# Optimization experiments

Hardware: AMD Instinct MI355X
Metric: run time of the kernel (lower is better)

The kernel has to match this reference:

```python
import jax, jax.numpy as jnp
import numpy as np

N = 100000
E = 1600000
H = 2   # heads
C = 64  # per-head channels
NEG_SLOPE = 0.2


def setup_inputs() -> dict:
    key = jax.random.key(0)
    ks = jax.random.split(key, 12)
    s = 0.05
    return {
        "logits": jax.random.normal(ks[0], (N, 40), jnp.float32),
        "features": jax.random.normal(ks[1], (N, 256), jnp.float32),
        "edge_index": jax.random.randint(ks[2], (2, E), 0, N, jnp.int32),
        "W_feat": jax.random.normal(ks[3], (256, 128), jnp.float32) * s,
        "b_feat": jnp.zeros((128,), jnp.float32),
        "W0": jax.random.normal(ks[4], (168, 128), jnp.float32) * s,
        "att_src0": jax.random.normal(ks[5], (H, C), jnp.float32) * s,
        "att_dst0": jax.random.normal(ks[6], (H, C), jnp.float32) * s,
        "bias0": jnp.zeros((128,), jnp.float32),
        "W1": jax.random.normal(ks[7], (128, 128), jnp.float32) * s,
        "att_src1": jax.random.normal(ks[8], (H, C), jnp.float32) * s,
        "att_dst1": jax.random.normal(ks[9], (H, C), jnp.float32) * s,
        "bias1": jnp.zeros((128,), jnp.float32),
        "W_out": jax.random.normal(ks[10], (128, 40), jnp.float32) * s,
        "b_out": jnp.zeros((40,), jnp.float32),
    }


def gat_conv(x, src, dst, W, att_src, att_dst, bias):
    # x: [N, F_in] -> h: [N, H, C]
    h = (x @ W).reshape(N, H, C)
    a_src = (h * att_src).sum(-1)  # [N, H]
    a_dst = (h * att_dst).sum(-1)  # [N, H]
    # per-edge attention logits, leaky relu
    e = jax.nn.leaky_relu(a_src[src] + a_dst[dst], NEG_SLOPE)  # [E+N, H]
    # segment softmax over incoming edges of each dst node
    e_max = jax.ops.segment_max(e, dst, num_segments=N)
    e_exp = jnp.exp(e - e_max[dst])
    denom = jax.ops.segment_sum(e_exp, dst, num_segments=N)
    alpha = e_exp / (denom[dst] + 1e-16)  # [E+N, H]
    # weighted message aggregation (scatter-add)
    msg = h[src] * alpha[:, :, None]  # [E+N, H, C]
    out = jax.ops.segment_sum(msg, dst, num_segments=N)
    return out.reshape(N, H * C) + bias


def reference(logits, features, edge_index, W_feat, b_feat,
              W0, att_src0, att_dst0, bias0,
              W1, att_src1, att_dst1, bias1,
              W_out, b_out):
    # input assembly: [logits | proj(features)]
    x = jnp.concatenate([logits, features @ W_feat + b_feat], axis=-1)  # [N,168]
    # add self loops (PyG GATConv default add_self_loops=True)
    loops = jnp.arange(N, dtype=edge_index.dtype)
    src = jnp.concatenate([edge_index[0], loops])
    dst = jnp.concatenate([edge_index[1], loops])
    x = gat_conv(x, src, dst, W0, att_src0, att_dst0, bias0)
    x = jax.nn.relu(x)  # relu between conv layers (dropout=0 / eval)
    x = gat_conv(x, src, dst, W1, att_src1, att_dst1, bias1)
    return x @ W_out + b_out  # [N, 40]
```

## Files before the change

### kernel.cpp

```cpp
#include <hip/hip_runtime.h>

#define NN 100000
#define EE 1600000
#define NBUCK ((NN + 255) >> 8)
#define CHUNK 8192
#define NPBLK ((EE + CHUNK - 1) / CHUNK)

typedef __attribute__((ext_vector_type(8))) short short8_t;
typedef __attribute__((ext_vector_type(4))) float f32x4;

static __device__ inline unsigned short f2bf(float f) {
    unsigned int u = __float_as_uint(f);
    u += 0x7FFFu + ((u >> 16) & 1u);
    return (unsigned short)(u >> 16);
}
static __device__ inline float bf2f(unsigned short h) {
    return __uint_as_float(((unsigned int)h) << 16);
}

__global__ __launch_bounds__(256) void part_count(const int* __restrict__ ei,
                                                  int* __restrict__ cnt) {
    __shared__ int h[NBUCK];
    for (int i = threadIdx.x; i < NBUCK; i += 256) h[i] = 0;
    __syncthreads();
    int e0 = blockIdx.x * CHUNK;
    int e1 = e0 + CHUNK; if (e1 > EE) e1 = EE;
    for (int e = e0 + threadIdx.x; e < e1; e += 256)
        atomicAdd(&h[ei[EE + e] >> 8], 1);
    __syncthreads();
    for (int i = threadIdx.x; i < NBUCK; i += 256)
        cnt[blockIdx.x * NBUCK + i] = h[i];
}

__global__ void part_scan(const int* __restrict__ cnt, int* __restrict__ base,
                          int* __restrict__ bbase) {
    __shared__ int tot[512];
    int b = threadIdx.x;
    int t = 0;
    if (b < NBUCK)
        for (int k = 0; k < NPBLK; ++k) t += cnt[k * NBUCK + b];
    tot[b] = t;
    __syncthreads();
    for (int off = 1; off < 512; off <<= 1) {
        int u = (b >= off) ? tot[b - off] : 0;
        __syncthreads();
        tot[b] += u;
        __syncthreads();
    }
    int excl = tot[b] - t;
    if (b < NBUCK) {
        bbase[b] = excl;
        int run = excl;
        for (int k = 0; k < NPBLK; ++k) {
            base[k * NBUCK + b] = run;
            run += cnt[k * NBUCK + b];
        }
    }
    if (b == 0) bbase[NBUCK] = EE;
}

__global__ __launch_bounds__(256) void part_scatter(const int* __restrict__ ei,
                                                    const int* __restrict__ base,
                                                    unsigned int* __restrict__ bbuf) {
    __shared__ int lcur[NBUCK];
    for (int i = threadIdx.x; i < NBUCK; i += 256)
        lcur[i] = base[blockIdx.x * NBUCK + i];
    __syncthreads();
    int e0 = blockIdx.x * CHUNK;
    int e1 = e0 + CHUNK; if (e1 > EE) e1 = EE;
    for (int e = e0 + threadIdx.x; e < e1; e += 256) {
        int s = ei[e], d = ei[EE + e];
        int pos = atomicAdd(&lcur[d >> 8], 1);
        bbuf[pos] = (unsigned int)s | ((unsigned int)(d & 255) << 24);
    }
}

__global__ __launch_bounds__(256) void csr_build(const unsigned int* __restrict__ bbuf,
                                                 const int* __restrict__ bbase,
                                                 int* __restrict__ row_ptr,
                                                 int* __restrict__ col) {
    __shared__ int hist[256];
    __shared__ int sc[256];
    __shared__ int lcur[256];
    int b = blockIdx.x;
    int t = threadIdx.x;
    int n0 = b << 8;
    int nCnt = NN - n0; if (nCnt > 256) nCnt = 256;
    int es = bbase[b], ee2 = bbase[b + 1];
    hist[t] = 0;
    __syncthreads();
    for (int i = es + t; i < ee2; i += 256)
        atomicAdd(&hist[bbuf[i] >> 24], 1);
    __syncthreads();
    int v = hist[t];
    sc[t] = v;
    __syncthreads();
    for (int off = 1; off < 256; off <<= 1) {
        int u = (t >= off) ? sc[t - off] : 0;
        __syncthreads();
        sc[t] += u;
        __syncthreads();
    }
    int excl = sc[t] - v;
    if (t < nCnt) row_ptr[n0 + t] = es + excl;
    if (b == 0 && t == 0) row_ptr[NN] = EE;
    lcur[t] = excl;
    __syncthreads();
    for (int i = es + t; i < ee2; i += 256) {
        unsigned int pk = bbuf[i];
        int lpos = atomicAdd(&lcur[pk >> 24], 1);
        col[es + lpos] = (int)(pk & 0x00FFFFFFu);
    }
}

__global__ void bsplit_kernel(const float* __restrict__ W, int ldw, int K, int N,
                              unsigned short* __restrict__ BThi,
                              unsigned short* __restrict__ BTlo,
                              int stride, int koff, int KPseg) {
    int k = blockIdx.x * 256 + threadIdx.x;
    int col = blockIdx.y;
    if (k >= KPseg) return;
    float v = (k < K && col < N) ? W[(size_t)k * ldw + col] : 0.f;
    unsigned short hi = f2bf(v);
    unsigned short lo = f2bf(v - bf2f(hi));
    BThi[(size_t)col * stride + koff + k] = hi;
    BTlo[(size_t)col * stride + koff + k] = lo;
}

__global__ void cvec_kernel(const float* __restrict__ b_feat,
                            const float* __restrict__ W0, float* __restrict__ cvec) {
    int j = threadIdx.x;
    float s = 0.f;
    for (int k = 0; k < 128; ++k) s += b_feat[k] * W0[(40 + k) * 128 + j];
    cvec[j] = s;
}

#define AHI 0
#define ALO 2048
#define BHI 4096
#define BLO 8192
template <int OUTBF16, int ABF16, int ATTN, int NCT>
__global__ __launch_bounds__(256) void mfma_gemm_kernel(
    const void* __restrict__ A1v, int lda1, int K1, int KP1,
    const float* __restrict__ A2, int lda2, int K2,
    int M,
    const unsigned short* __restrict__ BThi, const unsigned short* __restrict__ BTlo,
    int bstride, int KPtot,
    void* __restrict__ Cout, int ldc, int Nact, const float* __restrict__ bias,
    const float* __restrict__ att_src, const float* __restrict__ att_dst,
    float* __restrict__ a_srcO, float* __restrict__ a_dstO)
{
    __shared__ __align__(16) unsigned short lds[12288];
    const int t = threadIdx.x;
    const int w = t >> 6, lane = t & 63;
    const int row0 = blockIdx.x * 64;
    const int rbase = (w & 1) * 32;
    const int cbase = (NCT == 4) ? (w >> 1) * 64 : (w >> 1) * 32;

    f32x4 acc[2][NCT];
#pragma unroll
    for (int i = 0; i < 2; ++i)
#pragma unroll
        for (int j = 0; j < NCT; ++j) acc[i][j] = (f32x4){0.f, 0.f, 0.f, 0.f};

    const int arow = t >> 2;
    const int aslot = t & 3;
    const bool rowok = (row0 + arow) < M;
    const int aoff = arow * 32 + (((aslot ^ ((arow >> 1) & 3))) << 3);

    const int bc0 = t >> 2,         bs0 = t & 3;
    const int bc1 = (t + 256) >> 2, bs1 = (t + 256) & 3;
    const int bo0 = bc0 * 32 + ((bs0 ^ ((bc0 >> 1) & 3)) << 3);
    const int bo1 = bc1 * 32 + ((bs1 ^ ((bc1 >> 1) & 3)) << 3);

    float ra0[8], ra1[8];
    short8_t rab0, rab1;
    short8_t bh0a, bl0a, bh1a, bl1a;
    short8_t bh0b, bl0b, bh1b, bl1b;
    const short8_t zz = {0, 0, 0, 0, 0, 0, 0, 0};

#define LOADB_(k0_, H0, L0, H1, L1) {                                     \
        size_t g0_ = (size_t)bc0 * bstride + (k0_) + bs0 * 8;             \
        H0 = *(const short8_t*)&BThi[g0_];                                \
        L0 = *(const short8_t*)&BTlo[g0_];                                \
        if (NCT == 4) {                                                   \
            size_t g1_ = (size_t)bc1 * bstride + (k0_) + bs1 * 8;         \
            H1 = *(const short8_t*)&BThi[g1_];                            \
            L1 = *(const short8_t*)&BTlo[g1_];                            \
        }                                                                 \
    }

#define LOADA_(k0_, RA, RAB) {                                            \
        if (ABF16) {                                                      \
            int gk = (k0_) + aslot * 8;                                   \
            if (rowok && gk + 8 <= K1) {                                  \
                const unsigned short* Ab =                                \
                    (const unsigned short*)A1v + (size_t)(row0 + arow) * lda1; \
                RAB = *(const short8_t*)&Ab[gk];                          \
            } else RAB = zz;                                              \
        } else {                                                          \
            const float* Asrc; int gk, Klim;                              \
            if ((k0_) < KP1) {                                            \
                Asrc = (const float*)A1v + (size_t)(row0 + arow) * lda1;  \
                gk = (k0_) + aslot * 8; Klim = K1;                        \
            } else {                                                      \
                Asrc = A2 + (size_t)(row0 + arow) * lda2;                 \
                gk = (k0_) - KP1 + aslot * 8; Klim = K2;                  \
            }                                                             \
            if (rowok && gk + 8 <= Klim) {                                \
                float4 v0 = *(const float4*)(Asrc + gk);                  \
                float4 v1 = *(const float4*)(Asrc + gk + 4);              \
                RA[0] = v0.x; RA[1] = v0.y; RA[2] = v0.z; RA[3] = v0.w;   \
                RA[4] = v1.x; RA[5] = v1.y; RA[6] = v1.z; RA[7] = v1.w;   \
            } else {                                                      \
                for (int j_ = 0; j_ < 8; ++j_) RA[j_] = 0.f;              \
            }                                                             \
        }                                                                 \
    }

#define STAGE_(RA, RAB, H0, L0, H1, L1) {                                 \
        if (ABF16) {                                                      \
            *(short8_t*)&lds[AHI + aoff] = RAB;                           \
        } else {                                                          \
            short8_t vh_, vl_;                                            \
            for (int j_ = 0; j_ < 8; ++j_) {                              \
                unsigned short hi_ = f2bf(RA[j_]);                        \
                vh_[j_] = (short)hi_;                                     \
                vl_[j_] = (short)f2bf(RA[j_] - bf2f(hi_));                \
            }                                                             \
            *(short8_t*)&lds[AHI + aoff] = vh_;                           \
            *(short8_t*)&lds[ALO + aoff] = vl_;                           \
        }                                                                 \
        *(short8_t*)&lds[BHI + bo0] = H0;                                 \
        *(short8_t*)&lds[BLO + bo0] = L0;                                 \
        if (NCT == 4) {                                                   \
            *(short8_t*)&lds[BHI + bo1] = H1;                             \
            *(short8_t*)&lds[BLO + bo1] = L1;                             \
        }                                                                 \
    }

#define COMPUTE_() {                                                      \
        short8_t Ah[2], Al[2], Bh[NCT], Bl[NCT];                          \
        const int fslot = lane >> 4;                                      \
        for (int rt = 0; rt < 2; ++rt) {                                  \
            int r = rbase + rt * 16 + (lane & 15);                        \
            int off = r * 32 + ((fslot ^ ((r >> 1) & 3)) << 3);           \
            Ah[rt] = *(const short8_t*)&lds[AHI + off];                   \
            if (!ABF16) Al[rt] = *(const short8_t*)&lds[ALO + off];       \
        }                                                                 \
        for (int ct = 0; ct < NCT; ++ct) {                                \
            int c = cbase + ct * 16 + (lane & 15);                        \
            int off = c * 32 + ((fslot ^ ((c >> 1) & 3)) << 3);           \
            Bh[ct] = *(const short8_t*)&lds[BHI + off];                   \
            Bl[ct] = *(const short8_t*)&lds[BLO + off];                   \
        }                                                                 \
        for (int rt = 0; rt < 2; ++rt)                                    \
            for (int ct = 0; ct < NCT; ++ct) {                            \
                acc[rt][ct] = __builtin_amdgcn_mfma_f32_16x16x32_bf16(Ah[rt], Bh[ct], acc[rt][ct], 0, 0, 0); \
                acc[rt][ct] = __builtin_amdgcn_mfma_f32_16x16x32_bf16(Ah[rt], Bl[ct], acc[rt][ct], 0, 0, 0); \
                if (!ABF16)                                               \
                    acc[rt][ct] = __builtin_amdgcn_mfma_f32_16x16x32_bf16(Al[rt], Bh[ct], acc[rt][ct], 0, 0, 0); \
            }                                                             \
    }

    LOADA_(0, ra0, rab0);
    LOADB_(0, bh0a, bl0a, bh1a, bl1a);
    LOADA_(32, ra1, rab1);
    LOADB_(32, bh0b, bl0b, bh1b, bl1b);

    for (int k0 = 0; k0 < KPtot; k0 += 64) {
        STAGE_(ra0, rab0, bh0a, bl0a, bh1a, bl1a);
        __syncthreads();
        if (k0 + 64 < KPtot) {
            LOADA_(k0 + 64, ra0, rab0);
            LOADB_(k0 + 64, bh0a, bl0a, bh1a, bl1a);
        }
        COMPUTE_();
        __syncthreads();

        STAGE_(ra1, rab1, bh0b, bl0b, bh1b, bl1b);
        __syncthreads();
        if (k0 + 96 < KPtot) {
            LOADA_(k0 + 96, ra1, rab1);
            LOADB_(k0 + 96, bh0b, bl0b, bh1b, bl1b);
        }
        COMPUTE_();
        __syncthreads();
    }

#pragma unroll
    for (int rt = 0; rt < 2; ++rt) {
#pragma unroll
        for (int reg = 0; reg < 4; ++reg) {
            int r = row0 + rbase + rt * 16 + (lane >> 4) * 4 + reg;
            if (ATTN) {
                float ps = 0.f, pd = 0.f;
#pragma unroll
                for (int ct = 0; ct < NCT; ++ct) {
                    int c = cbase + ct * 16 + (lane & 15);
                    ps += acc[rt][ct][reg] * att_src[c];
                    pd += acc[rt][ct][reg] * att_dst[c];
                }
#pragma unroll
                for (int off = 1; off < 16; off <<= 1) {
                    ps += __shfl_xor(ps, off);
                    pd += __shfl_xor(pd, off);
                }
                if (r < M && (lane & 15) == 0) {
                    int head = w >> 1;
                    a_srcO[r * 2 + head] = ps;
                    a_dstO[r * 2 + head] = pd;
                }
            }
            if (r >= M) continue;
#pragma unroll
            for (int ct = 0; ct < NCT; ++ct) {
                int c = cbase + ct * 16 + (lane & 15);
                float v = acc[rt][ct][reg];
                if (bias) v += bias[c];
                if (OUTBF16) {
                    ((unsigned short*)Cout)[(size_t)r * 128 + c] = f2bf(v);
                } else {
                    if (c < Nact)
                        ((float*)Cout)[(size_t)r * ldc + c] = v;
                }
            }
        }
    }
#undef LOADA_
#undef LOADB_
#undef STAGE_
#undef COMPUTE_
}

template <int RELU, int OUTBF16>
__global__ void gat_agg_fused(const int* __restrict__ row_ptr, const int* __restrict__ col,
                              const float* __restrict__ a_src, const float* __restrict__ a_dst,
                              const unsigned short* __restrict__ hb,
                              const float* __restrict__ bias, void* __restrict__ out) {
    int wid = (blockIdx.x * 256 + threadIdx.x) >> 6;
    if (wid >= NN) return;
    int lane = threadIdx.x & 63;
    int hc = lane >> 5;
    const unsigned int* h2 = (const unsigned int*)hb;

    float2 ad = ((const float2*)a_dst)[wid];
    float2 asf = ((const float2*)a_src)[wid];
    float adh = hc ? ad.y : ad.x;
    float e0 = (hc ? asf.y : asf.x) + adh;
    e0 = e0 > 0.f ? e0 : 0.2f * e0;
    float w = __expf(e0);
    unsigned int hv = h2[wid * 64 + lane];
    float accx = w * __uint_as_float(hv << 16);
    float accy = w * __uint_as_float(hv & 0xFFFF0000u);
    float den = w;
    const int shbase = hc << 5;

    int rs = row_ptr[wid], re = row_ptr[wid + 1];
    for (int base = rs; base < re; base += 32) {
        int cnt = re - base;
        if (cnt > 32) cnt = 32;
        int eidx = lane & 31;
        int sL = 0;
        float wL = 0.f;
        if (eidx < cnt) {
            sL = col[base + eidx];
            float2 as = ((const float2*)a_src)[sL];
            float tt = (hc ? as.y : as.x) + adh;
            tt = tt > 0.f ? tt : 0.2f * tt;
            wL = __expf(tt);
        }
        int i = 0;
        for (; i + 8 <= cnt; i += 8) {
            int s[8];
            unsigned int g[8];
            float ws[8];
#pragma unroll
            for (int j = 0; j < 8; ++j) s[j] = __shfl(sL, shbase + i + j);
#pragma unroll
            for (int j = 0; j < 8; ++j) g[j] = h2[s[j] * 64 + lane];
#pragma unroll
            for (int j = 0; j < 8; ++j) ws[j] = __shfl(wL, shbase + i + j);
#pragma unroll
            for (int j = 0; j < 8; ++j) {
                accx += ws[j] * __uint_as_float(g[j] << 16);
                accy += ws[j] * __uint_as_float(g[j] & 0xFFFF0000u);
                den += ws[j];
            }
        }
        for (; i + 4 <= cnt; i += 4) {
            int s[4];
            unsigned int g[4];
            float ws[4];
#pragma unroll
            for (int j = 0; j < 4; ++j) s[j] = __shfl(sL, shbase + i + j);
#pragma unroll
            for (int j = 0; j < 4; ++j) g[j] = h2[s[j] * 64 + lane];
#pragma unroll
            for (int j = 0; j < 4; ++j) ws[j] = __shfl(wL, shbase + i + j);
#pragma unroll
            for (int j = 0; j < 4; ++j) {
                accx += ws[j] * __uint_as_float(g[j] << 16);
                accy += ws[j] * __uint_as_float(g[j] & 0xFFFF0000u);
                den += ws[j];
            }
        }
        for (; i < cnt; ++i) {
            int s = __shfl(sL, shbase + i);
            float ws = __shfl(wL, shbase + i);
            unsigned int hs = h2[s * 64 + lane];
            accx += ws * __uint_as_float(hs << 16);
            accy += ws * __uint_as_float(hs & 0xFFFF0000u);
            den += ws;
        }
    }
    float inv = 1.f / (den + 1e-16f);
    float2 b2 = ((const float2*)bias)[lane];
    float ox = accx * inv + b2.x;
    float oy = accy * inv + b2.y;
    if (RELU) { ox = fmaxf(ox, 0.f); oy = fmaxf(oy, 0.f); }
    if (OUTBF16) {
        unsigned int pk = (unsigned int)f2bf(ox) | ((unsigned int)f2bf(oy) << 16);
        ((unsigned int*)out)[wid * 64 + lane] = pk;
    } else {
        ((float2*)out)[wid * 64 + lane] = make_float2(ox, oy);
    }
}

extern "C" void kernel_launch(void* const* d_in, const int* in_sizes, int n_in,
                              void* d_out, int out_size, void* d_ws, size_t ws_size,
                              hipStream_t stream) {
    const float* logits   = (const float*)d_in[0];
    const float* features = (const float*)d_in[1];
    const int*   ei       = (const int*)d_in[2];
    const float* W_feat   = (const float*)d_in[3];
    const float* b_feat   = (const float*)d_in[4];
    const float* W0       = (const float*)d_in[5];
    const float* att_src0 = (const float*)d_in[6];
    const float* att_dst0 = (const float*)d_in[7];
    const float* bias0    = (const float*)d_in[8];
    const float* W1       = (const float*)d_in[9];
    const float* att_src1 = (const float*)d_in[10];
    const float* att_dst1 = (const float*)d_in[11];
    const float* bias1    = (const float*)d_in[12];
    const float* W_out    = (const float*)d_in[13];
    const float* b_out    = (const float*)d_in[14];
    float* out = (float*)d_out;

    float* agg    = (float*)d_ws;
    float* a_srcb = agg + (size_t)NN * 128;
    float* a_dstb = a_srcb + (size_t)NN * 2;
    float* Wc     = a_dstb + (size_t)NN * 2;
    float* cvec   = Wc + 256 * 128;
    unsigned short* hbuf = (unsigned short*)(cvec + 128);
    unsigned short* BT0hi = hbuf + (size_t)NN * 128;
    unsigned short* BT0lo = BT0hi + 128 * 320;
    unsigned short* BTbhi = BT0lo + 128 * 320;
    unsigned short* BTblo = BTbhi + 128 * 128;
    unsigned short* BT1hi = BTblo + 128 * 128;
    unsigned short* BT1lo = BT1hi + 128 * 128;
    unsigned short* BTohi = BT1lo + 128 * 128;
    unsigned short* BTolo = BTohi + 128 * 128;
    int* row_ptr = (int*)(BTolo + 128 * 128);
    int* colbuf  = row_ptr + NN + 1;
    int* cnt     = colbuf + EE;
    int* pbase   = cnt + NPBLK * NBUCK;
    int* bbase   = pbase + NPBLK * NBUCK;
    unsigned int* bbuf = (unsigned int*)agg;
    unsigned short* aggb = (unsigned short*)agg;

    dim3 blk(256);
    const int gemmGrid = (NN + 63) / 64;
    const int nodeWaveGrid = (NN + 3) / 4;

    part_count<<<dim3(NPBLK), blk, 0, stream>>>(ei, cnt);
    part_scan<<<dim3(1), dim3(512), 0, stream>>>(cnt, pbase, bbase);
    part_scatter<<<dim3(NPBLK), blk, 0, stream>>>(ei, pbase, bbuf);
    csr_build<<<dim3(NBUCK), blk, 0, stream>>>(bbuf, bbase, row_ptr, colbuf);

    bsplit_kernel<<<dim3(1, 128), blk, 0, stream>>>(W0, 128, 40, 128, BT0hi, BT0lo, 320, 0, 64);
    bsplit_kernel<<<dim3(1, 128), blk, 0, stream>>>(W0 + 40 * 128, 128, 128, 128, BTbhi, BTblo, 128, 0, 128);
    mfma_gemm_kernel<0, 0, 0, 4><<<dim3(4), blk, 0, stream>>>(
        W_feat, 128, 128, 128, nullptr, 0, 0, 256,
        BTbhi, BTblo, 128, 128, Wc, 128, 128, nullptr,
        nullptr, nullptr, nullptr, nullptr);
    cvec_kernel<<<dim3(1), dim3(128), 0, stream>>>(b_feat, W0, cvec);
    bsplit_kernel<<<dim3(1, 128), blk, 0, stream>>>(Wc, 128, 256, 128, BT0hi, BT0lo, 320, 64, 256);
    bsplit_kernel<<<dim3(1, 128), blk, 0, stream>>>(W1, 128, 128, 128, BT1hi, BT1lo, 128, 0, 128);
    bsplit_kernel<<<dim3(1, 128), blk, 0, stream>>>(W_out, 40, 128, 40, BTohi, BTolo, 128, 0, 128);

    mfma_gemm_kernel<1, 0, 1, 4><<<dim3(gemmGrid), blk, 0, stream>>>(
        logits, 40, 40, 64, features, 256, 256, NN,
        BT0hi, BT0lo, 320, 320, hbuf, 128, 128, cvec,
        att_src0, att_dst0, a_srcb, a_dstb);
    gat_agg_fused<1, 1><<<dim3(nodeWaveGrid), blk, 0, stream>>>(
        row_ptr, colbuf, a_srcb, a_dstb, hbuf, bias0, aggb);

    mfma_gemm_kernel<1, 1, 1, 4><<<dim3(gemmGrid), blk, 0, stream>>>(
        aggb, 128, 128, 128, nullptr, 0, 0, NN,
        BT1hi, BT1lo, 128, 128, hbuf, 128, 128, nullptr,
        att_src1, att_dst1, a_srcb, a_dstb);
    gat_agg_fused<0, 0><<<dim3(nodeWaveGrid), blk, 0, stream>>>(
        row_ptr, colbuf, a_srcb, a_dstb, hbuf, bias1, agg);

    mfma_gemm_kernel<0, 0, 0, 2><<<dim3(gemmGrid), blk, 0, stream>>>(
        agg, 128, 128, 128, nullptr, 0, 0, NN,
        BTohi, BTolo, 128, 128, out, 40, 40, b_out,
        nullptr, nullptr, nullptr, nullptr);
}
```

Baseline: 316.2 us.

## Drop LDS staging in GEMM and process two nodes per wave in aggregation

The MFMA GEMM loses its shared-memory staging and block barriers. Each wave now loads its A and B fragments straight from global memory into registers, owns a 32-row by 64-column tile, and double-buffers A across k-steps. The GAT aggregation kernel now handles two nodes per wave with 32 lanes each, reading 4 bf16 per lane and loop bounds set by the larger degree of the pair. The aim is to remove barrier and LDS overhead and to raise memory-level parallelism, at the cost of redundant global B reads across waves and idle lanes when paired nodes have very different degrees.

```diff
diff --git a/kernel.cpp b/kernel.cpp
--- a/kernel.cpp
+++ b/kernel.cpp
@@ -17,6 +17,7 @@
 static __device__ inline float bf2f(unsigned short h) {
     return __uint_as_float(((unsigned int)h) << 16);
 }
+static __device__ inline float u2f(unsigned int u) { return __uint_as_float(u); }
 
 __global__ __launch_bounds__(256) void part_count(const int* __restrict__ ei,
                                                   int* __restrict__ cnt) {
@@ -135,11 +136,7 @@
     cvec[j] = s;
 }
 
-#define AHI 0
-#define ALO 2048
-#define BHI 4096
-#define BLO 8192
-template <int OUTBF16, int ABF16, int ATTN, int NCT>
+template <int OUTBF16, int ABF16, int ATTN, int NCT, int COLSPLIT>
 __global__ __launch_bounds__(256) void mfma_gemm_kernel(
     const void* __restrict__ A1v, int lda1, int K1, int KP1,
     const float* __restrict__ A2, int lda2, int K2,
@@ -150,12 +147,14 @@
     const float* __restrict__ att_src, const float* __restrict__ att_dst,
     float* __restrict__ a_srcO, float* __restrict__ a_dstO)
 {
-    __shared__ __align__(16) unsigned short lds[12288];
-    const int t = threadIdx.x;
-    const int w = t >> 6, lane = t & 63;
-    const int row0 = blockIdx.x * 64;
-    const int rbase = (w & 1) * 32;
-    const int cbase = (NCT == 4) ? (w >> 1) * 64 : (w >> 1) * 32;
+    const int wv = (blockIdx.x * 256 + threadIdx.x) >> 6;
+    const int nRowWaves = M >> 5;
+    if (wv >= nRowWaves * COLSPLIT) return;
+    const int lane = threadIdx.x & 63;
+    const int fr = lane & 15;
+    const int fslot = lane >> 4;
+    const int row0 = (COLSPLIT == 2 ? (wv >> 1) : wv) * 32;
+    const int cbase = (COLSPLIT == 2 ? (wv & 1) * 64 : 0);
 
     f32x4 acc[2][NCT];
 #pragma unroll
@@ -163,141 +162,107 @@
 #pragma unroll
         for (int j = 0; j < NCT; ++j) acc[i][j] = (f32x4){0.f, 0.f, 0.f, 0.f};
 
-    const int arow = t >> 2;
-    const int aslot = t & 3;
-    const bool rowok = (row0 + arow) < M;
-    const int aoff = arow * 32 + (((aslot ^ ((arow >> 1) & 3))) << 3);
-
-    const int bc0 = t >> 2,         bs0 = t & 3;
-    const int bc1 = (t + 256) >> 2, bs1 = (t + 256) & 3;
-    const int bo0 = bc0 * 32 + ((bs0 ^ ((bc0 >> 1) & 3)) << 3);
-    const int bo1 = bc1 * 32 + ((bs1 ^ ((bc1 >> 1) & 3)) << 3);
-
-    float ra0[8], ra1[8];
-    short8_t rab0, rab1;
-    short8_t bh0a, bl0a, bh1a, bl1a;
-    short8_t bh0b, bl0b, bh1b, bl1b;
+    const unsigned short* Bhp[NCT];
+    const unsigned short* Blp[NCT];
+#pragma unroll
+    for (int ct = 0; ct < NCT; ++ct) {
+        size_t co = (size_t)(cbase + ct * 16 + fr) * bstride;
+        Bhp[ct] = BThi + co;
+        Blp[ct] = BTlo + co;
+    }
+    const unsigned short* Arow_b[2] = {nullptr, nullptr};
+    if (ABF16) {
+        Arow_b[0] = (const unsigned short*)A1v + (size_t)(row0 + fr) * lda1;
+        Arow_b[1] = Arow_b[0] + (size_t)16 * lda1;
+    }
+
     const short8_t zz = {0, 0, 0, 0, 0, 0, 0, 0};
-
-#define LOADB_(k0_, H0, L0, H1, L1) {                                     \
-        size_t g0_ = (size_t)bc0 * bstride + (k0_) + bs0 * 8;             \
-        H0 = *(const short8_t*)&BThi[g0_];                                \
-        L0 = *(const short8_t*)&BTlo[g0_];                                \
-        if (NCT == 4) {                                                   \
-            size_t g1_ = (size_t)bc1 * bstride + (k0_) + bs1 * 8;         \
-            H1 = *(const short8_t*)&BThi[g1_];                            \
-            L1 = *(const short8_t*)&BTlo[g1_];                            \
-        }                                                                 \
-    }
-
-#define LOADA_(k0_, RA, RAB) {                                            \
+    float raA[2][8], raB[2][8];
+    short8_t rabA[2], rabB[2];
+
+#define LOADA_(kk, RA, RAB) {                                             \
         if (ABF16) {                                                      \
-            int gk = (k0_) + aslot * 8;                                   \
-            if (rowok && gk + 8 <= K1) {                                  \
-                const unsigned short* Ab =                                \
-                    (const unsigned short*)A1v + (size_t)(row0 + arow) * lda1; \
-                RAB = *(const short8_t*)&Ab[gk];                          \
-            } else RAB = zz;                                              \
+            int gk = (kk) + fslot * 8;                                    \
+            _Pragma("unroll")                                             \
+            for (int rt = 0; rt < 2; ++rt)                                \
+                RAB[rt] = (gk + 8 <= K1) ? *(const short8_t*)&Arow_b[rt][gk] : zz; \
         } else {                                                          \
-            const float* Asrc; int gk, Klim;                              \
-            if ((k0_) < KP1) {                                            \
-                Asrc = (const float*)A1v + (size_t)(row0 + arow) * lda1;  \
-                gk = (k0_) + aslot * 8; Klim = K1;                        \
-            } else {                                                      \
-                Asrc = A2 + (size_t)(row0 + arow) * lda2;                 \
-                gk = (k0_) - KP1 + aslot * 8; Klim = K2;                  \
-            }                                                             \
-            if (rowok && gk + 8 <= Klim) {                                \
-                float4 v0 = *(const float4*)(Asrc + gk);                  \
-                float4 v1 = *(const float4*)(Asrc + gk + 4);              \
-                RA[0] = v0.x; RA[1] = v0.y; RA[2] = v0.z; RA[3] = v0.w;   \
-                RA[4] = v1.x; RA[5] = v1.y; RA[6] = v1.z; RA[7] = v1.w;   \
-            } else {                                                      \
-                for (int j_ = 0; j_ < 8; ++j_) RA[j_] = 0.f;              \
+            const float* Aseg; int kk2, Klim, ld_;                        \
+            if ((kk) < KP1) { Aseg = (const float*)A1v; kk2 = (kk); Klim = K1; ld_ = lda1; } \
+            else            { Aseg = A2; kk2 = (kk) - KP1; Klim = K2; ld_ = lda2; } \
+            int gk = kk2 + fslot * 8;                                     \
+            _Pragma("unroll")                                             \
+            for (int rt = 0; rt < 2; ++rt) {                              \
+                const float* p = Aseg + (size_t)(row0 + rt * 16 + fr) * ld_ + gk; \
+                if (gk + 8 <= Klim) {                                     \
+                    float4 v0 = *(const float4*)p;                        \
+                    float4 v1 = *(const float4*)(p + 4);                  \
+                    RA[rt][0] = v0.x; RA[rt][1] = v0.y; RA[rt][2] = v0.z; RA[rt][3] = v0.w; \
+                    RA[rt][4] = v1.x; RA[rt][5] = v1.y; RA[rt][6] = v1.z; RA[rt][7] = v1.w; \
+                } else {                                                  \
+                    _Pragma("unroll")                                     \
+                    for (int j_ = 0; j_ < 8; ++j_) RA[rt][j_] = 0.f;      \
+                }                                                         \
             }                                                             \
         }                                                                 \
     }
 
-#define STAGE_(RA, RAB, H0, L0, H1, L1) {                                 \
+#define GSTEP_(kk, RA, RAB, PREK, DOPRE, RAN, RABN) {                     \
+                                       \
+        short8_t bh[NCT], bl[NCT];                                        \
+        int ko_ = (kk) + fslot * 8;                                       \
+        _Pragma("unroll")                                                 \
+        for (int ct = 0; ct < NCT; ++ct) {                                \
+            bh[ct] = *(const short8_t*)&Bhp[ct][ko_];                     \
+            bl[ct] = *(const short8_t*)&Blp[ct][ko_];                     \
+        }                                                                 \
+              \
+        if (DOPRE) LOADA_(PREK, RAN, RABN);                               \
+                                                   \
+        short8_t ah[2], al[2];                                            \
         if (ABF16) {                                                      \
-            *(short8_t*)&lds[AHI + aoff] = RAB;                           \
+            ah[0] = RAB[0]; ah[1] = RAB[1];                               \
         } else {                                                          \
-            short8_t vh_, vl_;                                            \
-            for (int j_ = 0; j_ < 8; ++j_) {                              \
-                unsigned short hi_ = f2bf(RA[j_]);                        \
-                vh_[j_] = (short)hi_;                                     \
-                vl_[j_] = (short)f2bf(RA[j_] - bf2f(hi_));                \
+            _Pragma("unroll")                                             \
+            for (int rt = 0; rt < 2; ++rt) {                              \
+                _Pragma("unroll")                                         \
+                for (int j_ = 0; j_ < 8; ++j_) {                          \
+                    unsigned short hi_ = f2bf(RA[rt][j_]);                \
+                    ah[rt][j_] = (short)hi_;                              \
+                    al[rt][j_] = (short)f2bf(RA[rt][j_] - bf2f(hi_));     \
+                }                                                         \
             }                                                             \
-            *(short8_t*)&lds[AHI + aoff] = vh_;                           \
-            *(short8_t*)&lds[ALO + aoff] = vl_;                           \
         }                                                                 \
-        *(short8_t*)&lds[BHI + bo0] = H0;                                 \
-        *(short8_t*)&lds[BLO + bo0] = L0;                                 \
-        if (NCT == 4) {                                                   \
-            *(short8_t*)&lds[BHI + bo1] = H1;                             \
-            *(short8_t*)&lds[BLO + bo1] = L1;                             \
+        _Pragma("unroll")                                                 \
+        for (int rt = 0; rt < 2; ++rt) {                                  \
+            _Pragma("unroll")                                             \
+            for (int ct = 0; ct < NCT; ++ct) {                            \
+                acc[rt][ct] = __builtin_amdgcn_mfma_f32_16x16x32_bf16(ah[rt], bh[ct], acc[rt][ct], 0, 0, 0); \
+                acc[rt][ct] = __builtin_amdgcn_mfma_f32_16x16x32_bf16(ah[rt], bl[ct], acc[rt][ct], 0, 0, 0); \
+                if (!ABF16)                                               \
+                    acc[rt][ct] = __builtin_amdgcn_mfma_f32_16x16x32_bf16(al[rt], bh[ct], acc[rt][ct], 0, 0, 0); \
+            }                                                             \
         }                                                                 \
     }
 
-#define COMPUTE_() {                                                      \
-        short8_t Ah[2], Al[2], Bh[NCT], Bl[NCT];                          \
-        const int fslot = lane >> 4;                                      \
-        for (int rt = 0; rt < 2; ++rt) {                                  \
-            int r = rbase + rt * 16 + (lane & 15);                        \
-            int off = r * 32 + ((fslot ^ ((r >> 1) & 3)) << 3);           \
-            Ah[rt] = *(const short8_t*)&lds[AHI + off];                   \
-            if (!ABF16) Al[rt] = *(const short8_t*)&lds[ALO + off];       \
-        }                                                                 \
-        for (int ct = 0; ct < NCT; ++ct) {                                \
-            int c = cbase + ct * 16 + (lane & 15);                        \
-            int off = c * 32 + ((fslot ^ ((c >> 1) & 3)) << 3);           \
-            Bh[ct] = *(const short8_t*)&lds[BHI + off];                   \
-            Bl[ct] = *(const short8_t*)&lds[BLO + off];                   \
-        }                                                                 \
-        for (int rt = 0; rt < 2; ++rt)                                    \
-            for (int ct = 0; ct < NCT; ++ct) {                            \
-                acc[rt][ct] = __builtin_amdgcn_mfma_f32_16x16x32_bf16(Ah[rt], Bh[ct], acc[rt][ct], 0, 0, 0); \
-                acc[rt][ct] = __builtin_amdgcn_mfma_f32_16x16x32_bf16(Ah[rt], Bl[ct], acc[rt][ct], 0, 0, 0); \
-                if (!ABF16)                                               \
-                    acc[rt][ct] = __builtin_amdgcn_mfma_f32_16x16x32_bf16(Al[rt], Bh[ct], acc[rt][ct], 0, 0, 0); \
-            }                                                             \
-    }
-
-    LOADA_(0, ra0, rab0);
-    LOADB_(0, bh0a, bl0a, bh1a, bl1a);
-    LOADA_(32, ra1, rab1);
-    LOADB_(32, bh0b, bl0b, bh1b, bl1b);
-
+    LOADA_(0, raA, rabA);
     for (int k0 = 0; k0 < KPtot; k0 += 64) {
-        STAGE_(ra0, rab0, bh0a, bl0a, bh1a, bl1a);
-        __syncthreads();
-        if (k0 + 64 < KPtot) {
-            LOADA_(k0 + 64, ra0, rab0);
-            LOADB_(k0 + 64, bh0a, bl0a, bh1a, bl1a);
-        }
-        COMPUTE_();
-        __syncthreads();
-
-        STAGE_(ra1, rab1, bh0b, bl0b, bh1b, bl1b);
-        __syncthreads();
-        if (k0 + 96 < KPtot) {
-            LOADA_(k0 + 96, ra1, rab1);
-            LOADB_(k0 + 96, bh0b, bl0b, bh1b, bl1b);
-        }
-        COMPUTE_();
-        __syncthreads();
-    }
-
-#pragma unroll
-    for (int rt = 0; rt < 2; ++rt) {
-#pragma unroll
-        for (int reg = 0; reg < 4; ++reg) {
-            int r = row0 + rbase + rt * 16 + (lane >> 4) * 4 + reg;
-            if (ATTN) {
+        GSTEP_(k0, raA, rabA, k0 + 32, 1, raB, rabB);
+        GSTEP_(k0 + 32, raB, rabB, k0 + 64, (k0 + 64 < KPtot), raA, rabA);
+    }
+#undef LOADA_
+#undef GSTEP_
+
+    if (ATTN) {
+        const int head = wv & 1;
+#pragma unroll
+        for (int rt = 0; rt < 2; ++rt) {
+#pragma unroll
+            for (int reg = 0; reg < 4; ++reg) {
                 float ps = 0.f, pd = 0.f;
 #pragma unroll
                 for (int ct = 0; ct < NCT; ++ct) {
-                    int c = cbase + ct * 16 + (lane & 15);
+                    int c = cbase + ct * 16 + fr;
                     ps += acc[rt][ct][reg] * att_src[c];
                     pd += acc[rt][ct][reg] * att_dst[c];
                 }
@@ -306,16 +271,22 @@
                     ps += __shfl_xor(ps, off);
                     pd += __shfl_xor(pd, off);
                 }
-                if (r < M && (lane & 15) == 0) {
-                    int head = w >> 1;
+                if (fr == 0) {
+                    int r = row0 + rt * 16 + fslot * 4 + reg;
                     a_srcO[r * 2 + head] = ps;
                     a_dstO[r * 2 + head] = pd;
                 }
             }
-            if (r >= M) continue;
+        }
+    }
+#pragma unroll
+    for (int rt = 0; rt < 2; ++rt) {
+#pragma unroll
+        for (int reg = 0; reg < 4; ++reg) {
+            int r = row0 + rt * 16 + fslot * 4 + reg;
 #pragma unroll
             for (int ct = 0; ct < NCT; ++ct) {
-                int c = cbase + ct * 16 + (lane & 15);
+                int c = cbase + ct * 16 + fr;
                 float v = acc[rt][ct][reg];
                 if (bias) v += bias[c];
                 if (OUTBF16) {
@@ -327,103 +298,124 @@
             }
         }
     }
-#undef LOADA_
-#undef LOADB_
-#undef STAGE_
-#undef COMPUTE_
 }
 
 template <int RELU, int OUTBF16>
-__global__ void gat_agg_fused(const int* __restrict__ row_ptr, const int* __restrict__ col,
-                              const float* __restrict__ a_src, const float* __restrict__ a_dst,
-                              const unsigned short* __restrict__ hb,
-                              const float* __restrict__ bias, void* __restrict__ out) {
-    int wid = (blockIdx.x * 256 + threadIdx.x) >> 6;
-    if (wid >= NN) return;
+__global__ __launch_bounds__(256) void gat_agg_fused(
+    const int* __restrict__ row_ptr, const int* __restrict__ col,
+    const float* __restrict__ a_src, const float* __restrict__ a_dst,
+    const unsigned short* __restrict__ hb,
+    const float* __restrict__ bias, void* __restrict__ out)
+{
+    int wv = (blockIdx.x * 256 + threadIdx.x) >> 6;
     int lane = threadIdx.x & 63;
-    int hc = lane >> 5;
-    const unsigned int* h2 = (const unsigned int*)hb;
-
-    float2 ad = ((const float2*)a_dst)[wid];
-    float2 asf = ((const float2*)a_src)[wid];
-    float adh = hc ? ad.y : ad.x;
-    float e0 = (hc ? asf.y : asf.x) + adh;
+    int hl = lane >> 5;
+    int l5 = lane & 31;
+    int n = wv * 2 + hl;
+    if (n >= NN) return;
+    int hch = l5 >> 4;
+    const uint2* h4 = (const uint2*)hb;
+
+    float2 ad2 = ((const float2*)a_dst)[n];
+    float adh = hch ? ad2.y : ad2.x;
+    float2 as2 = ((const float2*)a_src)[n];
+    float e0 = (hch ? as2.y : as2.x) + adh;
     e0 = e0 > 0.f ? e0 : 0.2f * e0;
     float w = __expf(e0);
-    unsigned int hv = h2[wid * 64 + lane];
-    float accx = w * __uint_as_float(hv << 16);
-    float accy = w * __uint_as_float(hv & 0xFFFF0000u);
+    uint2 hv = h4[(size_t)n * 32 + l5];
+    float a0 = w * u2f(hv.x << 16);
+    float a1 = w * u2f(hv.x & 0xFFFF0000u);
+    float a2 = w * u2f(hv.y << 16);
+    float a3 = w * u2f(hv.y & 0xFFFF0000u);
     float den = w;
-    const int shbase = hc << 5;
-
-    int rs = row_ptr[wid], re = row_ptr[wid + 1];
-    for (int base = rs; base < re; base += 32) {
+
+    int rs = row_ptr[n], re = row_ptr[n + 1];
+    int deg = re - rs;
+    int degO = __shfl(deg, lane ^ 32);
+    int degm = deg > degO ? deg : degO;
+    int nbm = (degm + 15) >> 4;
+
+    for (int bi = 0; bi < nbm; ++bi) {
+        int base = rs + bi * 16;
         int cnt = re - base;
-        if (cnt > 32) cnt = 32;
-        int eidx = lane & 31;
+        cnt = cnt < 0 ? 0 : (cnt > 16 ? 16 : cnt);
+        int cntO = __shfl(cnt, lane ^ 32);
+        int cntm = cnt > cntO ? cnt : cntO;
+        int j16 = l5 & 15;
         int sL = 0;
         float wL = 0.f;
-        if (eidx < cnt) {
-            sL = col[base + eidx];
+        if (j16 < cnt) {
+            sL = col[base + j16];
             float2 as = ((const float2*)a_src)[sL];
-            float tt = (hc ? as.y : as.x) + adh;
+            float tt = (hch ? as.y : as.x) + adh;
             tt = tt > 0.f ? tt : 0.2f * tt;
             wL = __expf(tt);
         }
+        const int sb = hl << 5;
+        const int wb = sb + (hch << 4);
         int i = 0;
-        for (; i + 8 <= cnt; i += 8) {
-            int s[8];
-            unsigned int g[8];
-            float ws[8];
-#pragma unroll
-            for (int j = 0; j < 8; ++j) s[j] = __shfl(sL, shbase + i + j);
-#pragma unroll
-            for (int j = 0; j < 8; ++j) g[j] = h2[s[j] * 64 + lane];
-#pragma unroll
-            for (int j = 0; j < 8; ++j) ws[j] = __shfl(wL, shbase + i + j);
+        for (; i + 8 <= cntm; i += 8) {
+            int s[8]; uint2 g[8]; float ws[8];
+#pragma unroll
+            for (int j = 0; j < 8; ++j) s[j] = __shfl(sL, sb + i + j);
+#pragma unroll
+            for (int j = 0; j < 8; ++j) g[j] = h4[(size_t)s[j] * 32 + l5];
+#pragma unroll
+            for (int j = 0; j < 8; ++j) ws[j] = __shfl(wL, wb + i + j);
 #pragma unroll
             for (int j = 0; j < 8; ++j) {
-                accx += ws[j] * __uint_as_float(g[j] << 16);
-                accy += ws[j] * __uint_as_float(g[j] & 0xFFFF0000u);
+                a0 += ws[j] * u2f(g[j].x << 16);
+                a1 += ws[j] * u2f(g[j].x & 0xFFFF0000u);
+                a2 += ws[j] * u2f(g[j].y << 16);
+                a3 += ws[j] * u2f(g[j].y & 0xFFFF0000u);
                 den += ws[j];
             }
         }
-        for (; i + 4 <= cnt; i += 4) {
-            int s[4];
-            unsigned int g[4];
-            float ws[4];
-#pragma unroll
-            for (int j = 0; j < 4; ++j) s[j] = __shfl(sL, shbase + i + j);
-#pragma unroll
-            for (int j = 0; j < 4; ++j) g[j] = h2[s[j] * 64 + lane];
-#pragma unroll
-            for (int j = 0; j < 4; ++j) ws[j] = __shfl(wL, shbase + i + j);
+        for (; i + 4 <= cntm; i += 4) {
+            int s[4]; uint2 g[4]; float ws[4];
+#pragma unroll
+            for (int j = 0; j < 4; ++j) s[j] = __shfl(sL, sb + i + j);
+#pragma unroll
+            for (int j = 0; j < 4; ++j) g[j] = h4[(size_t)s[j] * 32 + l5];
+#pragma unroll
+            for (int j = 0; j < 4; ++j) ws[j] = __shfl(wL, wb + i + j);
 #pragma unroll
             for (int j = 0; j < 4; ++j) {
-                accx += ws[j] * __uint_as_float(g[j] << 16);
-                accy += ws[j] * __uint_as_float(g[j] & 0xFFFF0000u);
+                a0 += ws[j] * u2f(g[j].x << 16);
+                a1 += ws[j] * u2f(g[j].x & 0xFFFF0000u);
+                a2 += ws[j] * u2f(g[j].y << 16);
+                a3 += ws[j] * u2f(g[j].y & 0xFFFF0000u);
                 den += ws[j];
             }
         }
-        for (; i < cnt; ++i) {
-            int s = __shfl(sL, shbase + i);
-            float ws = __shfl(wL, shbase + i);
-            unsigned int hs = h2[s * 64 + lane];
-            accx += ws * __uint_as_float(hs << 16);
-            accy += ws * __uint_as_float(hs & 0xFFFF0000u);
+        for (; i < cntm; ++i) {
+            int s = __shfl(sL, sb + i);
+            float ws = __shfl(wL, wb + i);
+            uint2 g = h4[(size_t)s * 32 + l5];
+            a0 += ws * u2f(g.x << 16);
+            a1 += ws * u2f(g.x & 0xFFFF0000u);
+            a2 += ws * u2f(g.y << 16);
+            a3 += ws * u2f(g.y & 0xFFFF0000u);
             den += ws;
         }
     }
     float inv = 1.f / (den + 1e-16f);
-    float2 b2 = ((const float2*)bias)[lane];
-    float ox = accx * inv + b2.x;
-    float oy = accy * inv + b2.y;
-    if (RELU) { ox = fmaxf(ox, 0.f); oy = fmaxf(oy, 0.f); }
+    float4 b4 = ((const float4*)bias)[l5];
+    float o0 = a0 * inv + b4.x;
+    float o1 = a1 * inv + b4.y;
+    float o2 = a2 * inv + b4.z;
+    float o3 = a3 * inv + b4.w;
+    if (RELU) {
+        o0 = fmaxf(o0, 0.f); o1 = fmaxf(o1, 0.f);
+        o2 = fmaxf(o2, 0.f); o3 = fmaxf(o3, 0.f);
+    }
     if (OUTBF16) {
-        unsigned int pk = (unsigned int)f2bf(ox) | ((unsigned int)f2bf(oy) << 16);
-        ((unsigned int*)out)[wid * 64 + lane] = pk;
+        uint2 pk;
+        pk.x = (unsigned int)f2bf(o0) | ((unsigned int)f2bf(o1) << 16);
+        pk.y = (unsigned int)f2bf(o2) | ((unsigned int)f2bf(o3) << 16);
+        ((uint2*)out)[(size_t)n * 32 + l5] = pk;
     } else {
-        ((float2*)out)[wid * 64 + lane] = make_float2(ox, oy);
+        ((float4*)out)[(size_t)n * 32 + l5] = make_float4(o0, o1, o2, o3);
     }
 }
 
@@ -470,8 +462,9 @@
     unsigned short* aggb = (unsigned short*)agg;
 
     dim3 blk(256);
-    const int gemmGrid = (NN + 63) / 64;
-    const int nodeWaveGrid = (NN + 3) / 4;
+    const int gemmGrid2 = ((NN / 32) * 2 + 3) / 4;
+    const int gemmGrid1 = ((NN / 32) + 3) / 4;
+    const int aggGrid = (NN / 2 + 3) / 4;
 
     part_count<<<dim3(NPBLK), blk, 0, stream>>>(ei, cnt);
     part_scan<<<dim3(1), dim3(512), 0, stream>>>(cnt, pbase, bbase);
@@ -480,7 +473,7 @@
 
     bsplit_kernel<<<dim3(1, 128), blk, 0, stream>>>(W0, 128, 40, 128, BT0hi, BT0lo, 320, 0, 64);
     bsplit_kernel<<<dim3(1, 128), blk, 0, stream>>>(W0 + 40 * 128, 128, 128, 128, BTbhi, BTblo, 128, 0, 128);
-    mfma_gemm_kernel<0, 0, 0, 4><<<dim3(4), blk, 0, stream>>>(
+    mfma_gemm_kernel<0, 0, 0, 4, 2><<<dim3(4), blk, 0, stream>>>(
         W_feat, 128, 128, 128, nullptr, 0, 0, 256,
         BTbhi, BTblo, 128, 128, Wc, 128, 128, nullptr,
         nullptr, nullptr, nullptr, nullptr);
@@ -489,21 +482,21 @@
     bsplit_kernel<<<dim3(1, 128), blk, 0, stream>>>(W1, 128, 128, 128, BT1hi, BT1lo, 128, 0, 128);
     bsplit_kernel<<<dim3(1, 128), blk, 0, stream>>>(W_out, 40, 128, 40, BTohi, BTolo, 128, 0, 128);
 
-    mfma_gemm_kernel<1, 0, 1, 4><<<dim3(gemmGrid), blk, 0, stream>>>(
+    mfma_gemm_kernel<1, 0, 1, 4, 2><<<dim3(gemmGrid2), blk, 0, stream>>>(
         logits, 40, 40, 64, features, 256, 256, NN,
         BT0hi, BT0lo, 320, 320, hbuf, 128, 128, cvec,
         att_src0, att_dst0, a_srcb, a_dstb);
-    gat_agg_fused<1, 1><<<dim3(nodeWaveGrid), blk, 0, stream>>>(
+    gat_agg_fused<1, 1><<<dim3(aggGrid), blk, 0, stream>>>(
         row_ptr, colbuf, a_srcb, a_dstb, hbuf, bias0, aggb);
 
-    mfma_gemm_kernel<1, 1, 1, 4><<<dim3(gemmGrid), blk, 0, stream>>>(
+    mfma_gemm_kernel<1, 1, 1, 4, 2><<<dim3(gemmGrid2), blk, 0, stream>>>(
         aggb, 128, 128, 128, nullptr, 0, 0, NN,
         BT1hi, BT1lo, 128, 128, hbuf, 128, 128, nullptr,
         att_src1, att_dst1, a_srcb, a_dstb);
-    gat_agg_fused<0, 0><<<dim3(nodeWaveGrid), blk, 0, stream>>>(
+    gat_agg_fused<0, 0><<<dim3(aggGrid), blk, 0, stream>>>(
         row_ptr, colbuf, a_srcb, a_dstb, hbuf, bias1, agg);
 
-    mfma_gemm_kernel<0, 0, 0, 2><<<dim3(gemmGrid), blk, 0, stream>>>(
+    mfma_gemm_kernel<0, 0, 0, 3, 1><<<dim3(gemmGrid1), blk, 0, stream>>>(
         agg, 128, 128, 128, nullptr, 0, 0, NN,
         BTohi, BTolo, 128, 128, out, 40, 40, b_out,
         nullptr, nullptr, nullptr, nullptr);
```

Result: slower. 388.2 us (+22.8%).
